# Kernel optimization log

Hardware: AMD Instinct MI355X
Metric: run time of the kernel (lower is better)

## Reference

```python
import jax, jax.numpy as jnp
import numpy as np

N_NODES = 65536
N_EDGES = 1048576
F_IN = 128
HEADS = 4
HID = 64
N_GRAPHS = 1024
NODES_PER_GRAPH = N_NODES // N_GRAPHS
EPS = 1e-5
NEG_SLOPE = 0.2


def setup_inputs() -> dict:
    key = jax.random.key(0)
    ks = jax.random.split(key, 8)
    x = jax.random.normal(ks[0], (N_NODES, F_IN), dtype=jnp.float32)
    edge_index = jax.random.randint(ks[1], (2, N_EDGES), 0, N_NODES, dtype=jnp.int64)
    batch = (jnp.arange(N_NODES, dtype=jnp.int64) // NODES_PER_GRAPH)
    s = 1.0 / np.sqrt(F_IN)
    w_l = jax.random.normal(ks[2], (HEADS * HID, F_IN), dtype=jnp.float32) * s
    w_r = jax.random.normal(ks[3], (HEADS * HID, F_IN), dtype=jnp.float32) * s
    att = jax.random.normal(ks[4], (HEADS, HID), dtype=jnp.float32) * (1.0 / np.sqrt(HID))
    return {
        "x": x,
        "edge_index": edge_index,
        "batch": batch,
        "num_graphs": N_GRAPHS,
        "bn_gamma": jnp.ones((F_IN,), jnp.float32),
        "bn_beta": jnp.zeros((F_IN,), jnp.float32),
        "w_l": w_l,
        "b_l": jnp.zeros((HEADS * HID,), jnp.float32),
        "w_r": w_r,
        "b_r": jnp.zeros((HEADS * HID,), jnp.float32),
        "att": att,
        "bias": jnp.zeros((HID,), jnp.float32),
    }


def reference(x, edge_index, batch, num_graphs, bn_gamma, bn_beta,
              w_l, b_l, w_r, b_r, att, bias):
    N = x.shape[0]
    H, C = att.shape
    # BatchNorm1d (training-mode: batch stats, biased variance)
    mean = jnp.mean(x, axis=0)
    var = jnp.var(x, axis=0)
    xn = (x - mean) * jax.lax.rsqrt(var + EPS) * bn_gamma + bn_beta
    # GATv2Conv: separate src/dst linear transforms
    xs = (xn @ w_l.T + b_l).reshape(N, H, C)
    xd = (xn @ w_r.T + b_r).reshape(N, H, C)
    # add self-loops (PyG default)
    loop = jnp.arange(N, dtype=edge_index.dtype)
    src = jnp.concatenate([edge_index[0], loop])
    dst = jnp.concatenate([edge_index[1], loop])
    # per-edge messages and GATv2 attention logits
    msg = xs[src]                               # [E, H, C]
    e = jax.nn.leaky_relu(msg + xd[dst], NEG_SLOPE)
    logits = jnp.einsum('ehc,hc->eh', e, att)    # [E, H]
    # segment-wise (per-destination) softmax
    m = jax.ops.segment_max(logits, dst, num_segments=N)
    p = jnp.exp(logits - m[dst])
    s = jax.ops.segment_sum(p, dst, num_segments=N)
    alpha = p / s[dst]                           # [E, H]
    # scatter-aggregate weighted messages
    out = jax.ops.segment_sum(alpha[:, :, None] * msg, dst, num_segments=N)  # [N,H,C]
    out = out.mean(axis=1) + bias                # concat=False -> mean over heads
    out = jax.nn.elu(out)
    return out.reshape(num_graphs, -1, C)
```

## Files before the change

### kernel.cpp

```cpp
#include <hip/hip_runtime.h>
#include <hip/hip_bf16.h>

#define N_NODES 65536
#define N_EDGES 1048576
#define F_IN    128
#define HEADS   4
#define HID     64
#define NHID    256
#define NBUCK   1024
#define BCAP    2048

typedef float fx4 __attribute__((ext_vector_type(4)));
typedef short bf16x8 __attribute__((ext_vector_type(8)));
typedef float f32x4 __attribute__((ext_vector_type(4)));
typedef float f32x2 __attribute__((ext_vector_type(2)));

typedef __attribute__((address_space(1))) const unsigned as1_cuint;
typedef __attribute__((address_space(3))) unsigned as3_uint;

__device__ inline unsigned short f2bf(float f) {
    unsigned u = __float_as_uint(f);
    u += 0x7fff + ((u >> 16) & 1);
    return (unsigned short)(u >> 16);
}
__device__ inline float bflo(unsigned w) { return __uint_as_float(w << 16); }
__device__ inline float bfhi(unsigned w) { return __uint_as_float(w & 0xffff0000u); }

template <int CTRL>
__device__ inline float dpp_add(float x) {
    int y = __builtin_amdgcn_update_dpp(0, __float_as_int(x), CTRL, 0xf, 0xf, true);
    return x + __int_as_float(y);
}

__global__ __launch_bounds__(256) void k_bn_stats(const float* __restrict__ x,
                                                  float* __restrict__ sums,
                                                  unsigned short* __restrict__ xhi) {
    const int t = threadIdx.x;
    const int lane = t & 63;
    const int w = t >> 6;
    const int wid = blockIdx.x * 4 + w;
    float s0 = 0.f, s1 = 0.f, q0 = 0.f, q1 = 0.f;
    for (int i = 0; i < 64; ++i) {
        int r = wid + i * 1024;
        float2 v = *(const float2*)(x + (size_t)r * F_IN + lane * 2);
        s0 += v.x; q0 += v.x * v.x;
        s1 += v.y; q1 += v.y * v.y;
        unsigned short h0 = f2bf(v.x), h1 = f2bf(v.y);
        int slot = (lane >> 2) ^ (r & 7);
        int idx = r * 64 + slot * 4 + (lane & 3);
        ((unsigned*)xhi)[idx] = (unsigned)h0 | ((unsigned)h1 << 16);
    }
    __shared__ float sh[4][128];
    sh[w][lane * 2] = s0; sh[w][lane * 2 + 1] = s1;
    __syncthreads();
    if (t < 128) atomicAdd(&sums[t], sh[0][t] + sh[1][t] + sh[2][t] + sh[3][t]);
    __syncthreads();
    sh[w][lane * 2] = q0; sh[w][lane * 2 + 1] = q1;
    __syncthreads();
    if (t < 128) atomicAdd(&sums[128 + t], sh[0][t] + sh[1][t] + sh[2][t] + sh[3][t]);
}

__global__ __launch_bounds__(256) void k_prep_w(const float* __restrict__ w_l,
                                                const float* __restrict__ b_l,
                                                const float* __restrict__ w_r,
                                                const float* __restrict__ b_r,
                                                const float* __restrict__ gamma,
                                                const float* __restrict__ beta,
                                                const float* __restrict__ sums,
                                                unsigned short* __restrict__ Whi,
                                                float* __restrict__ bp) {
    const int t = threadIdx.x;
    const int lane = t & 63;
    const int o = blockIdx.x * 4 + (t >> 6);
    const int k0 = lane * 2, k1 = k0 + 1;
    const float invN = 1.0f / N_NODES;
    float mean0 = sums[k0] * invN, mean1 = sums[k1] * invN;
    float var0 = sums[128 + k0] * invN - mean0 * mean0;
    float var1 = sums[128 + k1] * invN - mean1 * mean1;
    float sc0 = gamma[k0] * rsqrtf(var0 + 1e-5f);
    float sc1 = gamma[k1] * rsqrtf(var1 + 1e-5f);
    float sh0 = beta[k0] - mean0 * sc0;
    float sh1 = beta[k1] - mean1 * sc1;
    const float* wrow = (o < NHID) ? (w_l + (size_t)o * F_IN)
                                   : (w_r + (size_t)(o - NHID) * F_IN);
    float bo = (o < NHID) ? b_l[o] : b_r[o - NHID];
    float2 wv = *(const float2*)(wrow + lane * 2);
    float w0 = wv.x * sc0, w1 = wv.y * sc1;
    int slot = (lane >> 2) ^ (o & 7);
    int idx = o * 64 + slot * 4 + (lane & 3);
    ((unsigned*)Whi)[idx] = (unsigned)f2bf(w0) | ((unsigned)f2bf(w1) << 16);
    float part = sh0 * wv.x + sh1 * wv.y;
    #pragma unroll
    for (int m = 1; m < 64; m <<= 1) part += __shfl_xor(part, m, 64);
    if (lane == 0) bp[o] = bo + part;
}

__global__ __launch_bounds__(512) void k_gemm_mfma(const unsigned short* __restrict__ xhi,
                                                   const unsigned short* __restrict__ Whi,
                                                   const float* __restrict__ bp,
                                                   unsigned short* __restrict__ xs_bf,
                                                   unsigned short* __restrict__ xd_bf) {
    __shared__ __align__(16) char lds[65536];
    const int t = threadIdx.x;
    const int bid = blockIdx.x;
    const int mb = (bid & 7) * 64 + ((bid >> 3) >> 2);
    const int nb = (bid >> 3) & 3;
    const int m0 = mb * 128, n0 = nb * 128;
    {
        const unsigned* srcs[2] = {
            (const unsigned*)(xhi + (size_t)m0 * 128),
            (const unsigned*)(Whi + (size_t)n0 * 128)};
        #pragma unroll
        for (int c = 0; c < 2; ++c) {
            #pragma unroll
            for (int q = 0; q < 4; ++q) {
                int i = (q * 512 + t) * 4;
                __builtin_amdgcn_global_load_lds(
                    (as1_cuint*)(srcs[c] + i),
                    (as3_uint*)(lds + c * 32768 + i * 4),
                    16, 0, 0);
            }
        }
    }
    __syncthreads();
    const int wvi = t >> 6, lane = t & 63;
    const int wm = wvi >> 2, wn = wvi & 3;
    const int lg = lane >> 4, lr = lane & 15;
    f32x4 acc[4][2] = {};
    #pragma unroll
    for (int ks = 0; ks < 4; ++ks) {
        bf16x8 ah[4], bh[2];
        #pragma unroll
        for (int mi = 0; mi < 4; ++mi) {
            int r = wm * 64 + mi * 16 + lr;
            int off = r * 256 + ((((ks << 2) + lg) ^ (r & 7)) << 4);
            ah[mi] = *(const bf16x8*)(lds + off);
        }
        #pragma unroll
        for (int nj = 0; nj < 2; ++nj) {
            int r = wn * 32 + nj * 16 + lr;
            int off = r * 256 + ((((ks << 2) + lg) ^ (r & 7)) << 4);
            bh[nj] = *(const bf16x8*)(lds + 32768 + off);
        }
        #pragma unroll
        for (int mi = 0; mi < 4; ++mi)
            #pragma unroll
            for (int nj = 0; nj < 2; ++nj)
                acc[mi][nj] = __builtin_amdgcn_mfma_f32_16x16x32_bf16(ah[mi], bh[nj], acc[mi][nj], 0, 0, 0);
    }
    unsigned short* outp = (n0 < NHID) ? xs_bf : xd_bf;
    const int ncol0 = n0 & 255;
    #pragma unroll
    for (int nj = 0; nj < 2; ++nj) {
        int nc = wn * 32 + nj * 16 + lr;
        float bcol = bp[n0 + nc];
        #pragma unroll
        for (int mi = 0; mi < 4; ++mi) {
            #pragma unroll
            for (int r = 0; r < 4; ++r) {
                int m = m0 + wm * 64 + mi * 16 + lg * 4 + r;
                outp[(size_t)m * NHID + ncol0 + nc] = f2bf(acc[mi][nj][r] + bcol);
            }
        }
    }
}

__global__ __launch_bounds__(256) void k_coarse(const int* __restrict__ ei,
                                                int* __restrict__ ccnt,
                                                unsigned* __restrict__ cbuf) {
    __shared__ int cnt[NBUCK];
    __shared__ int base[NBUCK];
    const int t = threadIdx.x;
    for (int i = t; i < NBUCK; i += 256) cnt[i] = 0;
    __syncthreads();
    const int e0 = blockIdx.x * 4096;
    int myrank[16];
    #pragma unroll
    for (int k = 0; k < 16; ++k) {
        int d = ei[N_EDGES + e0 + k * 256 + t];
        myrank[k] = atomicAdd(&cnt[d >> 6], 1);
    }
    __syncthreads();
    for (int i = t; i < NBUCK; i += 256)
        base[i] = (i << 11) + atomicAdd(&ccnt[i], cnt[i]);
    __syncthreads();
    #pragma unroll
    for (int k = 0; k < 16; ++k) {
        int e = e0 + k * 256 + t;
        int s = ei[e];
        int d = ei[N_EDGES + e];
        unsigned pos = (unsigned)(base[d >> 6] + myrank[k]);
        if ((pos >> 11) == (unsigned)(d >> 6))
            cbuf[pos] = (unsigned)s | ((unsigned)(d & 63) << 16);
    }
}

__global__ __launch_bounds__(256) void k_fine(const unsigned* __restrict__ cbuf,
                                              const int* __restrict__ ccnt,
                                              int* __restrict__ counts,
                                              int* __restrict__ row_start,
                                              int* __restrict__ csr) {
    __shared__ int nc[64];
    __shared__ int rowst[64];
    __shared__ int red[256];
    const int t = threadIdx.x;
    const int b = blockIdx.x;
    if (t < 64) nc[t] = 0;
    int s = 0;
    for (int i = t; i < b; i += 256) s += ccnt[i];
    red[t] = s;
    __syncthreads();
    for (int off = 128; off > 0; off >>= 1) {
        if (t < off) red[t] += red[t + off];
        __syncthreads();
    }
    const int cnt = min(ccnt[b], BCAP);
    const unsigned* p = cbuf + (size_t)b * BCAP;
    unsigned w2[8];
    int rank[8];
    #pragma unroll
    for (int k = 0; k < 8; ++k) {
        int e = t + k * 256;
        if (e < cnt) {
            w2[k] = p[e];
            rank[k] = atomicAdd(&nc[(w2[k] >> 16) & 63], 1);
        }
    }
    __syncthreads();
    if (t < 64) {
        int v = nc[t];
        counts[b * 64 + t] = v;
        int inc = v;
        #pragma unroll
        for (int off = 1; off < 64; off <<= 1) {
            int n = __shfl_up(inc, off, 64);
            if (t >= off) inc += n;
        }
        int rs = red[0] + inc - v;
        row_start[b * 64 + t] = rs;
        rowst[t] = rs;
    }
    __syncthreads();
    #pragma unroll
    for (int k = 0; k < 8; ++k) {
        int e = t + k * 256;
        if (e < cnt) {
            int d = (w2[k] >> 16) & 63;
            csr[rowst[d] + rank[k]] = (int)(w2[k] & 0xffffu);
        }
    }
}

__global__ __launch_bounds__(256) void k_aggregate(const unsigned short* __restrict__ xs_bf,
                                                   const unsigned short* __restrict__ xd_bf,
                                                   const int* __restrict__ row_start,
                                                   const int* __restrict__ counts,
                                                   const int* __restrict__ csr,
                                                   const float* __restrict__ att,
                                                   const float* __restrict__ bias,
                                                   float* __restrict__ out) {
    const int t = threadIdx.x;
    const int lane = t & 63;
    const int node  = __builtin_amdgcn_readfirstlane(blockIdx.x * 4 + (t >> 6));
    const int start = __builtin_amdgcn_readfirstlane(row_start[node]);
    const int deg   = __builtin_amdgcn_readfirstlane(counts[node]);
    const int total = deg + 1;

    const float CATT = 0.6f * 1.44269504088896f;
    f32x2 att01, att23, xd01, xd23;
    {
        float4 a = *(const float4*)(att + lane * 4);
        att01.x = CATT * a.x; att01.y = CATT * a.y;
        att23.x = CATT * a.z; att23.y = CATT * a.w;
        uint2 xw = *(const uint2*)(xd_bf + (size_t)node * NHID + lane * 4);
        xd01.x = bflo(xw.x); xd01.y = bfhi(xw.x);
        xd23.x = bflo(xw.y); xd23.y = bfhi(xw.y);
    }

    const char* xsb = (const char*)xs_bf;
    const unsigned voff = (unsigned)lane * 8;
    float ssumA = 0.f, ssumB = 0.f;
    f32x2 accA01 = {0.f, 0.f}, accA23 = {0.f, 0.f};
    f32x2 accB01 = {0.f, 0.f}, accB23 = {0.f, 0.f};

#define LDX(S) (*(const uint2*)(xsb + (((size_t)(unsigned)(S)) << 9) + voff))
#define PROC(U, GUARD, KOFF, SS, A01, A23) {                                   \
        f32x2 c01, c23;                                                        \
        c01.x = bflo((U).x); c01.y = bfhi((U).x);                              \
        c23.x = bflo((U).y); c23.y = bfhi((U).y);                              \
        f32x2 sv01 = c01 + xd01, sv23 = c23 + xd23;                            \
        f32x2 dA2 = att01 * c01 + att23 * c23;                                 \
        f32x2 a01v, a23v;                                                      \
        a01v.x = fabsf(sv01.x); a01v.y = fabsf(sv01.y);                        \
        a23v.x = fabsf(sv23.x); a23v.y = fabsf(sv23.y);                        \
        f32x2 dB2 = att01 * a01v + att23 * a23v;                               \
        float d_ = fmaf(0.66666667f, dB2.x + dB2.y, dA2.x + dA2.y);            \
        d_ = dpp_add<0xB1>(d_);                                                \
        d_ = dpp_add<0x4E>(d_);                                                \
        d_ = dpp_add<0x141>(d_);                                               \
        d_ = dpp_add<0x140>(d_);                         \
        if (GUARD && j + (KOFF) >= cnt) d_ = -1e30f;                           \
        float p_ = __builtin_amdgcn_exp2f(d_);                                 \
        SS += p_;                                                              \
        f32x2 p2 = {p_, p_};                                                   \
        A01 += p2 * c01; A23 += p2 * c23; }

    for (int base = 0; base < total; base += 64) {
        const int cnt = __builtin_amdgcn_readfirstlane(min(64, total - base));
        int item = base + lane;
        int idx = node;
        if ((unsigned)(item - 1) < (unsigned)deg)
            idx = csr[start + item - 1];
        uint2 c0 = LDX(__builtin_amdgcn_readlane(idx, 0));
        uint2 c1 = LDX(__builtin_amdgcn_readlane(idx, 1));
        uint2 c2 = LDX(__builtin_amdgcn_readlane(idx, 2));
        uint2 c3 = LDX(__builtin_amdgcn_readlane(idx, 3));
        int j = 0;
        for (; j + 4 <= cnt; j += 4) {
            uint2 u0 = c0, u1 = c1, u2 = c2, u3 = c3;
            if (j + 4 < cnt) {
                c0 = LDX(__builtin_amdgcn_readlane(idx, j + 4));
                c1 = LDX(__builtin_amdgcn_readlane(idx, j + 5));
                c2 = LDX(__builtin_amdgcn_readlane(idx, j + 6));
                c3 = LDX(__builtin_amdgcn_readlane(idx, j + 7));
            }
            PROC(u0, false, 0, ssumA, accA01, accA23)
            PROC(u1, false, 1, ssumB, accB01, accB23)
            PROC(u2, false, 2, ssumA, accA01, accA23)
            PROC(u3, false, 3, ssumB, accB01, accB23)
        }
        if (j < cnt) {
            uint2 u0 = c0, u1 = c1, u2 = c2, u3 = c3;
            PROC(u0, true, 0, ssumA, accA01, accA23)
            PROC(u1, true, 1, ssumB, accB01, accB23)
            PROC(u2, true, 2, ssumA, accA01, accA23)
            PROC(u3, true, 3, ssumB, accB01, accB23)
        }
    }
#undef PROC
#undef LDX

    float ssum = ssumA + ssumB;
    f32x2 acc01 = accA01 + accB01;
    f32x2 acc23 = accA23 + accB23;

    float inv = __builtin_amdgcn_rcpf(ssum);
    float r0 = acc01.x * inv, r1 = acc01.y * inv;
    float r2 = acc23.x * inv, r3 = acc23.y * inv;
    r0 += __shfl_xor(r0, 16, 64); r0 += __shfl_xor(r0, 32, 64);
    r1 += __shfl_xor(r1, 16, 64); r1 += __shfl_xor(r1, 32, 64);
    r2 += __shfl_xor(r2, 16, 64); r2 += __shfl_xor(r2, 32, 64);
    r3 += __shfl_xor(r3, 16, 64); r3 += __shfl_xor(r3, 32, 64);
    if (lane < 16) {
        float4 b4 = *(const float4*)(bias + lane * 4);
        float o0 = r0 * 0.25f + b4.x;
        float o1 = r1 * 0.25f + b4.y;
        float o2 = r2 * 0.25f + b4.z;
        float o3 = r3 * 0.25f + b4.w;
        o0 = (o0 > 0.f) ? o0 : __builtin_amdgcn_exp2f(o0 * 1.44269504f) - 1.0f;
        o1 = (o1 > 0.f) ? o1 : __builtin_amdgcn_exp2f(o1 * 1.44269504f) - 1.0f;
        o2 = (o2 > 0.f) ? o2 : __builtin_amdgcn_exp2f(o2 * 1.44269504f) - 1.0f;
        o3 = (o3 > 0.f) ? o3 : __builtin_amdgcn_exp2f(o3 * 1.44269504f) - 1.0f;
        float4 o = {o0, o1, o2, o3};
        *(float4*)(out + (size_t)node * HID + lane * 4) = o;
    }
}

extern "C" void kernel_launch(void* const* d_in, const int* in_sizes, int n_in,
                              void* d_out, int out_size, void* d_ws, size_t ws_size,
                              hipStream_t stream) {
    const float* x     = (const float*)d_in[0];
    const int*   ei    = (const int*)d_in[1];
    const float* gamma = (const float*)d_in[4];
    const float* beta  = (const float*)d_in[5];
    const float* w_l   = (const float*)d_in[6];
    const float* b_l   = (const float*)d_in[7];
    const float* w_r   = (const float*)d_in[8];
    const float* b_r   = (const float*)d_in[9];
    const float* att   = (const float*)d_in[10];
    const float* bias  = (const float*)d_in[11];
    float* out = (float*)d_out;

    char* ws = (char*)d_ws;
    unsigned short* xs_bf = (unsigned short*)ws;
    unsigned short* xd_bf = xs_bf + (size_t)N_NODES * NHID;
    unsigned short* xhi   = xd_bf + (size_t)N_NODES * NHID;
    unsigned short* Whi   = xhi + (size_t)N_NODES * F_IN;
    float* bp      = (float*)(Whi + 512 * F_IN);
    float* sums    = bp + 512;
    int* ccnt      = (int*)(sums + 256);
    int* counts    = ccnt + NBUCK;
    int* row_start = counts + N_NODES;
    int* csr       = row_start + N_NODES;
    unsigned* cbuf = (unsigned*)(csr + N_EDGES);

    (void)hipMemsetAsync(sums, 0, (256 + NBUCK) * sizeof(float), stream);

    k_bn_stats<<<256, 256, 0, stream>>>(x, sums, xhi);
    k_prep_w<<<128, 256, 0, stream>>>(w_l, b_l, w_r, b_r, gamma, beta, sums, Whi, bp);
    k_gemm_mfma<<<2048, 512, 0, stream>>>(xhi, Whi, bp, xs_bf, xd_bf);

    k_coarse<<<N_EDGES / 4096, 256, 0, stream>>>(ei, ccnt, cbuf);
    k_fine<<<NBUCK, 256, 0, stream>>>(cbuf, ccnt, counts, row_start, csr);

    k_aggregate<<<N_NODES / 4, 256, 0, stream>>>(xs_bf, xd_bf, row_start, counts, csr,
                                                 att, bias, out);
}
```

Baseline: 155.7 us.

## Merge independent graph-build kernels into BN-stats and GEMM launches

Runs the coarse edge bucketing in extra blocks of the BN-stats kernel and the fine CSR build in extra blocks of the MFMA GEMM kernel. This cuts the launch count from six kernels to four and lets the independent edge-sorting work fill the GPU alongside the dense stages. The fine stage now runs with 512 threads and 64KB of static LDS per block, which may lower occupancy for those blocks. The BN-stats blocks also reserve more shared memory than they need.

```diff
diff --git a/kernel.cpp b/kernel.cpp
--- a/kernel.cpp
+++ b/kernel.cpp
@@ -32,32 +32,63 @@
     return x + __int_as_float(y);
 }
 
-__global__ __launch_bounds__(256) void k_bn_stats(const float* __restrict__ x,
-                                                  float* __restrict__ sums,
-                                                  unsigned short* __restrict__ xhi) {
+__global__ __launch_bounds__(256) void k_front(const float* __restrict__ x,
+                                               float* __restrict__ sums,
+                                               unsigned short* __restrict__ xhi,
+                                               const int* __restrict__ ei,
+                                               int* __restrict__ ccnt,
+                                               unsigned* __restrict__ cbuf) {
+    __shared__ int smem[2048];
     const int t = threadIdx.x;
-    const int lane = t & 63;
-    const int w = t >> 6;
-    const int wid = blockIdx.x * 4 + w;
-    float s0 = 0.f, s1 = 0.f, q0 = 0.f, q1 = 0.f;
-    for (int i = 0; i < 64; ++i) {
-        int r = wid + i * 1024;
-        float2 v = *(const float2*)(x + (size_t)r * F_IN + lane * 2);
-        s0 += v.x; q0 += v.x * v.x;
-        s1 += v.y; q1 += v.y * v.y;
-        unsigned short h0 = f2bf(v.x), h1 = f2bf(v.y);
-        int slot = (lane >> 2) ^ (r & 7);
-        int idx = r * 64 + slot * 4 + (lane & 3);
-        ((unsigned*)xhi)[idx] = (unsigned)h0 | ((unsigned)h1 << 16);
+    if (blockIdx.x < 256) {
+        const int lane = t & 63;
+        const int w = t >> 6;
+        const int wid = blockIdx.x * 4 + w;
+        float* sh = (float*)smem;
+        float s0 = 0.f, s1 = 0.f, q0 = 0.f, q1 = 0.f;
+        for (int i = 0; i < 64; ++i) {
+            int r = wid + i * 1024;
+            float2 v = *(const float2*)(x + (size_t)r * F_IN + lane * 2);
+            s0 += v.x; q0 += v.x * v.x;
+            s1 += v.y; q1 += v.y * v.y;
+            unsigned short h0 = f2bf(v.x), h1 = f2bf(v.y);
+            int slot = (lane >> 2) ^ (r & 7);
+            int idx = r * 64 + slot * 4 + (lane & 3);
+            ((unsigned*)xhi)[idx] = (unsigned)h0 | ((unsigned)h1 << 16);
+        }
+        sh[w * 128 + lane * 2] = s0; sh[w * 128 + lane * 2 + 1] = s1;
+        __syncthreads();
+        if (t < 128) atomicAdd(&sums[t], sh[t] + sh[128 + t] + sh[256 + t] + sh[384 + t]);
+        __syncthreads();
+        sh[w * 128 + lane * 2] = q0; sh[w * 128 + lane * 2 + 1] = q1;
+        __syncthreads();
+        if (t < 128) atomicAdd(&sums[128 + t], sh[t] + sh[128 + t] + sh[256 + t] + sh[384 + t]);
+    } else {
+        int* cnt  = smem;
+        int* base = smem + 1024;
+        for (int i = t; i < NBUCK; i += 256) cnt[i] = 0;
+        __syncthreads();
+        const int e0 = (blockIdx.x - 256) * 4096;
+        int myrank[16];
+        #pragma unroll
+        for (int k = 0; k < 16; ++k) {
+            int d = ei[N_EDGES + e0 + k * 256 + t];
+            myrank[k] = atomicAdd(&cnt[d >> 6], 1);
+        }
+        __syncthreads();
+        for (int i = t; i < NBUCK; i += 256)
+            base[i] = (i << 11) + atomicAdd(&ccnt[i], cnt[i]);
+        __syncthreads();
+        #pragma unroll
+        for (int k = 0; k < 16; ++k) {
+            int e = e0 + k * 256 + t;
+            int s = ei[e];
+            int d = ei[N_EDGES + e];
+            unsigned pos = (unsigned)(base[d >> 6] + myrank[k]);
+            if ((pos >> 11) == (unsigned)(d >> 6))
+                cbuf[pos] = (unsigned)s | ((unsigned)(d & 63) << 16);
+        }
     }
-    __shared__ float sh[4][128];
-    sh[w][lane * 2] = s0; sh[w][lane * 2 + 1] = s1;
-    __syncthreads();
-    if (t < 128) atomicAdd(&sums[t], sh[0][t] + sh[1][t] + sh[2][t] + sh[3][t]);
-    __syncthreads();
-    sh[w][lane * 2] = q0; sh[w][lane * 2 + 1] = q1;
-    __syncthreads();
-    if (t < 128) atomicAdd(&sums[128 + t], sh[0][t] + sh[1][t] + sh[2][t] + sh[3][t]);
 }
 
 __global__ __launch_bounds__(256) void k_prep_w(const float* __restrict__ w_l,
@@ -95,158 +126,128 @@
     if (lane == 0) bp[o] = bo + part;
 }
 
-__global__ __launch_bounds__(512) void k_gemm_mfma(const unsigned short* __restrict__ xhi,
+__global__ __launch_bounds__(512) void k_gemm_fine(const unsigned short* __restrict__ xhi,
                                                    const unsigned short* __restrict__ Whi,
                                                    const float* __restrict__ bp,
                                                    unsigned short* __restrict__ xs_bf,
-                                                   unsigned short* __restrict__ xd_bf) {
+                                                   unsigned short* __restrict__ xd_bf,
+                                                   const unsigned* __restrict__ cbuf,
+                                                   const int* __restrict__ ccnt,
+                                                   int* __restrict__ counts,
+                                                   int* __restrict__ row_start,
+                                                   int* __restrict__ csr) {
     __shared__ __align__(16) char lds[65536];
     const int t = threadIdx.x;
-    const int bid = blockIdx.x;
-    const int mb = (bid & 7) * 64 + ((bid >> 3) >> 2);
-    const int nb = (bid >> 3) & 3;
-    const int m0 = mb * 128, n0 = nb * 128;
-    {
-        const unsigned* srcs[2] = {
-            (const unsigned*)(xhi + (size_t)m0 * 128),
-            (const unsigned*)(Whi + (size_t)n0 * 128)};
-        #pragma unroll
-        for (int c = 0; c < 2; ++c) {
-            #pragma unroll
-            for (int q = 0; q < 4; ++q) {
-                int i = (q * 512 + t) * 4;
-                __builtin_amdgcn_global_load_lds(
-                    (as1_cuint*)(srcs[c] + i),
-                    (as3_uint*)(lds + c * 32768 + i * 4),
-                    16, 0, 0);
-            }
-        }
-    }
-    __syncthreads();
-    const int wvi = t >> 6, lane = t & 63;
-    const int wm = wvi >> 2, wn = wvi & 3;
-    const int lg = lane >> 4, lr = lane & 15;
-    f32x4 acc[4][2] = {};
-    #pragma unroll
-    for (int ks = 0; ks < 4; ++ks) {
-        bf16x8 ah[4], bh[2];
-        #pragma unroll
-        for (int mi = 0; mi < 4; ++mi) {
-            int r = wm * 64 + mi * 16 + lr;
-            int off = r * 256 + ((((ks << 2) + lg) ^ (r & 7)) << 4);
-            ah[mi] = *(const bf16x8*)(lds + off);
-        }
+    if (blockIdx.x < 2048) {
+        const int bid = blockIdx.x;
+        const int mb = (bid & 7) * 64 + ((bid >> 3) >> 2);
+        const int nb = (bid >> 3) & 3;
+        const int m0 = mb * 128, n0 = nb * 128;
+        {
+            const unsigned* srcs[2] = {
+                (const unsigned*)(xhi + (size_t)m0 * 128),
+                (const unsigned*)(Whi + (size_t)n0 * 128)};
+            #pragma unroll
+            for (int c = 0; c < 2; ++c) {
+                #pragma unroll
+                for (int q = 0; q < 4; ++q) {
+                    int i = (q * 512 + t) * 4;
+                    __builtin_amdgcn_global_load_lds(
+                        (as1_cuint*)(srcs[c] + i),
+                        (as3_uint*)(lds + c * 32768 + i * 4),
+                        16, 0, 0);
+                }
+            }
+        }
+        __syncthreads();
+        const int wvi = t >> 6, lane = t & 63;
+        const int wm = wvi >> 2, wn = wvi & 3;
+        const int lg = lane >> 4, lr = lane & 15;
+        f32x4 acc[4][2] = {};
+        #pragma unroll
+        for (int ks = 0; ks < 4; ++ks) {
+            bf16x8 ah[4], bh[2];
+            #pragma unroll
+            for (int mi = 0; mi < 4; ++mi) {
+                int r = wm * 64 + mi * 16 + lr;
+                int off = r * 256 + ((((ks << 2) + lg) ^ (r & 7)) << 4);
+                ah[mi] = *(const bf16x8*)(lds + off);
+            }
+            #pragma unroll
+            for (int nj = 0; nj < 2; ++nj) {
+                int r = wn * 32 + nj * 16 + lr;
+                int off = r * 256 + ((((ks << 2) + lg) ^ (r & 7)) << 4);
+                bh[nj] = *(const bf16x8*)(lds + 32768 + off);
+            }
+            #pragma unroll
+            for (int mi = 0; mi < 4; ++mi)
+                #pragma unroll
+                for (int nj = 0; nj < 2; ++nj)
+                    acc[mi][nj] = __builtin_amdgcn_mfma_f32_16x16x32_bf16(ah[mi], bh[nj], acc[mi][nj], 0, 0, 0);
+        }
+        unsigned short* outp = (n0 < NHID) ? xs_bf : xd_bf;
+        const int ncol0 = n0 & 255;
         #pragma unroll
         for (int nj = 0; nj < 2; ++nj) {
-            int r = wn * 32 + nj * 16 + lr;
-            int off = r * 256 + ((((ks << 2) + lg) ^ (r & 7)) << 4);
-            bh[nj] = *(const bf16x8*)(lds + 32768 + off);
-        }
-        #pragma unroll
-        for (int mi = 0; mi < 4; ++mi)
-            #pragma unroll
-            for (int nj = 0; nj < 2; ++nj)
-                acc[mi][nj] = __builtin_amdgcn_mfma_f32_16x16x32_bf16(ah[mi], bh[nj], acc[mi][nj], 0, 0, 0);
-    }
-    unsigned short* outp = (n0 < NHID) ? xs_bf : xd_bf;
-    const int ncol0 = n0 & 255;
-    #pragma unroll
-    for (int nj = 0; nj < 2; ++nj) {
-        int nc = wn * 32 + nj * 16 + lr;
-        float bcol = bp[n0 + nc];
-        #pragma unroll
-        for (int mi = 0; mi < 4; ++mi) {
-            #pragma unroll
-            for (int r = 0; r < 4; ++r) {
-                int m = m0 + wm * 64 + mi * 16 + lg * 4 + r;
-                outp[(size_t)m * NHID + ncol0 + nc] = f2bf(acc[mi][nj][r] + bcol);
-            }
-        }
-    }
-}
-
-__global__ __launch_bounds__(256) void k_coarse(const int* __restrict__ ei,
-                                                int* __restrict__ ccnt,
-                                                unsigned* __restrict__ cbuf) {
-    __shared__ int cnt[NBUCK];
-    __shared__ int base[NBUCK];
-    const int t = threadIdx.x;
-    for (int i = t; i < NBUCK; i += 256) cnt[i] = 0;
-    __syncthreads();
-    const int e0 = blockIdx.x * 4096;
-    int myrank[16];
-    #pragma unroll
-    for (int k = 0; k < 16; ++k) {
-        int d = ei[N_EDGES + e0 + k * 256 + t];
-        myrank[k] = atomicAdd(&cnt[d >> 6], 1);
-    }
-    __syncthreads();
-    for (int i = t; i < NBUCK; i += 256)
-        base[i] = (i << 11) + atomicAdd(&ccnt[i], cnt[i]);
-    __syncthreads();
-    #pragma unroll
-    for (int k = 0; k < 16; ++k) {
-        int e = e0 + k * 256 + t;
-        int s = ei[e];
-        int d = ei[N_EDGES + e];
-        unsigned pos = (unsigned)(base[d >> 6] + myrank[k]);
-        if ((pos >> 11) == (unsigned)(d >> 6))
-            cbuf[pos] = (unsigned)s | ((unsigned)(d & 63) << 16);
-    }
-}
-
-__global__ __launch_bounds__(256) void k_fine(const unsigned* __restrict__ cbuf,
-                                              const int* __restrict__ ccnt,
-                                              int* __restrict__ counts,
-                                              int* __restrict__ row_start,
-                                              int* __restrict__ csr) {
-    __shared__ int nc[64];
-    __shared__ int rowst[64];
-    __shared__ int red[256];
-    const int t = threadIdx.x;
-    const int b = blockIdx.x;
-    if (t < 64) nc[t] = 0;
-    int s = 0;
-    for (int i = t; i < b; i += 256) s += ccnt[i];
-    red[t] = s;
-    __syncthreads();
-    for (int off = 128; off > 0; off >>= 1) {
-        if (t < off) red[t] += red[t + off];
-        __syncthreads();
-    }
-    const int cnt = min(ccnt[b], BCAP);
-    const unsigned* p = cbuf + (size_t)b * BCAP;
-    unsigned w2[8];
-    int rank[8];
-    #pragma unroll
-    for (int k = 0; k < 8; ++k) {
-        int e = t + k * 256;
-        if (e < cnt) {
-            w2[k] = p[e];
-            rank[k] = atomicAdd(&nc[(w2[k] >> 16) & 63], 1);
-        }
-    }
-    __syncthreads();
-    if (t < 64) {
-        int v = nc[t];
-        counts[b * 64 + t] = v;
-        int inc = v;
-        #pragma unroll
-        for (int off = 1; off < 64; off <<= 1) {
-            int n = __shfl_up(inc, off, 64);
-            if (t >= off) inc += n;
-        }
-        int rs = red[0] + inc - v;
-        row_start[b * 64 + t] = rs;
-        rowst[t] = rs;
-    }
-    __syncthreads();
-    #pragma unroll
-    for (int k = 0; k < 8; ++k) {
-        int e = t + k * 256;
-        if (e < cnt) {
-            int d = (w2[k] >> 16) & 63;
-            csr[rowst[d] + rank[k]] = (int)(w2[k] & 0xffffu);
+            int nc2 = wn * 32 + nj * 16 + lr;
+            float bcol = bp[n0 + nc2];
+            #pragma unroll
+            for (int mi = 0; mi < 4; ++mi) {
+                #pragma unroll
+                for (int r = 0; r < 4; ++r) {
+                    int m = m0 + wm * 64 + mi * 16 + lg * 4 + r;
+                    outp[(size_t)m * NHID + ncol0 + nc2] = f2bf(acc[mi][nj][r] + bcol);
+                }
+            }
+        }
+    } else {
+        const int b = blockIdx.x - 2048;
+        int* nc    = (int*)lds;
+        int* rowst = nc + 64;
+        int* red   = rowst + 64;
+        if (t < 64) nc[t] = 0;
+        int s = 0;
+        for (int i = t; i < b; i += 512) s += ccnt[i];
+        red[t] = s;
+        __syncthreads();
+        for (int off = 256; off > 0; off >>= 1) {
+            if (t < off) red[t] += red[t + off];
+            __syncthreads();
+        }
+        const int cnt = min(ccnt[b], BCAP);
+        const unsigned* p = cbuf + (size_t)b * BCAP;
+        unsigned w2[4];
+        int rank[4];
+        #pragma unroll
+        for (int k = 0; k < 4; ++k) {
+            int e = t + k * 512;
+            if (e < cnt) {
+                w2[k] = p[e];
+                rank[k] = atomicAdd(&nc[(w2[k] >> 16) & 63], 1);
+            }
+        }
+        __syncthreads();
+        if (t < 64) {
+            int v = nc[t];
+            counts[b * 64 + t] = v;
+            int inc = v;
+            #pragma unroll
+            for (int off = 1; off < 64; off <<= 1) {
+                int n = __shfl_up(inc, off, 64);
+                if (t >= off) inc += n;
+            }
+            int rs = red[0] + inc - v;
+            row_start[b * 64 + t] = rs;
+            rowst[t] = rs;
+        }
+        __syncthreads();
+        #pragma unroll
+        for (int k = 0; k < 4; ++k) {
+            int e = t + k * 512;
+            if (e < cnt) {
+                int d = (w2[k] >> 16) & 63;
+                csr[rowst[d] + rank[k]] = (int)(w2[k] & 0xffffu);
+            }
         }
     }
 }
@@ -396,13 +397,10 @@
 
     (void)hipMemsetAsync(sums, 0, (256 + NBUCK) * sizeof(float), stream);
 
-    k_bn_stats<<<256, 256, 0, stream>>>(x, sums, xhi);
+    k_front<<<512, 256, 0, stream>>>(x, sums, xhi, ei, ccnt, cbuf);
     k_prep_w<<<128, 256, 0, stream>>>(w_l, b_l, w_r, b_r, gamma, beta, sums, Whi, bp);
-    k_gemm_mfma<<<2048, 512, 0, stream>>>(xhi, Whi, bp, xs_bf, xd_bf);
-
-    k_coarse<<<N_EDGES / 4096, 256, 0, stream>>>(ei, ccnt, cbuf);
-    k_fine<<<NBUCK, 256, 0, stream>>>(cbuf, ccnt, counts, row_start, csr);
-
+    k_gemm_fine<<<3072, 512, 0, stream>>>(xhi, Whi, bp, xs_bf, xd_bf,
+                                          cbuf, ccnt, counts, row_start, csr);
     k_aggregate<<<N_NODES / 4, 256, 0, stream>>>(xs_bf, xd_bf, row_start, counts, csr,
                                                  att, bias, out);
 }
```

Result: faster. 145.2 us (median of 2 runs) (-6.7%).
